# Kernel optimization log

Hardware: AMD Instinct MI355X
Metric: run time of the kernel (lower is better)

## Reference

```python
import jax, jax.numpy as jnp
import numpy as np

D_IN = 1024
D_OUT = 1024
NUM_HEADS = 16
HEAD_DIM = D_OUT // NUM_HEADS


def setup_inputs() -> dict:
    key = jax.random.key(0)
    ks = jax.random.split(key, 6)
    s = 1.0 / np.sqrt(D_IN)
    x = jax.random.normal(ks[0], (2, 2048, D_IN), dtype=jnp.float32)
    Wq = jax.random.uniform(ks[1], (D_IN, D_OUT), jnp.float32, -s, s)
    Wk = jax.random.uniform(ks[2], (D_IN, D_OUT), jnp.float32, -s, s)
    Wv = jax.random.uniform(ks[3], (D_IN, D_OUT), jnp.float32, -s, s)
    Wo = jax.random.uniform(ks[4], (D_OUT, D_OUT), jnp.float32, -s, s)
    bo = jax.random.uniform(ks[5], (D_OUT,), jnp.float32, -s, s)
    return {"x": x, "Wq": Wq, "Wk": Wk, "Wv": Wv, "Wo": Wo, "bo": bo}


def reference(x, Wq, Wk, Wv, Wo, bo):
    b, T, _ = x.shape
    # projections -> [b, heads, T, head_dim]
    def split_heads(y):
        return y.reshape(b, T, NUM_HEADS, HEAD_DIM).transpose(0, 2, 1, 3)
    q = split_heads(x @ Wq)
    k = split_heads(x @ Wk)
    v = split_heads(x @ Wv)
    scores = jnp.einsum("bhqd,bhkd->bhqk", q, k)  # [b,h,T,T]
    causal = jnp.triu(jnp.ones((T, T), dtype=bool), k=1)
    scores = jnp.where(causal, -jnp.inf, scores)
    weights = jax.nn.softmax(scores / np.sqrt(HEAD_DIM), axis=-1)
    # dropout p=0.0 (eval) -> identity
    ctx = jnp.einsum("bhqk,bhkd->bhqd", weights, v)
    ctx = ctx.transpose(0, 2, 1, 3).reshape(b, T, D_OUT)
    return ctx @ Wo + bo
```

## Files before the change

kernel.cpp:

```cpp
#include <hip/hip_runtime.h>
#include <hip/hip_bf16.h>
#include <math.h>

using f32x4  = __attribute__((ext_vector_type(4)))  float;
using f32x16 = __attribute__((ext_vector_type(16))) float;
using s16x8  = __attribute__((ext_vector_type(8)))  short;
using s16x4  = __attribute__((ext_vector_type(4)))  short;

#define HD 64
#define NH 16
#define TT 2048
#define DIN 1024
#define NB 2
#define M_TOK (NB*TT)
#define PADK 40
#define PSTR 36

__device__ __forceinline__ ushort f2b(float f) {
  union { float f; unsigned u; } v; v.f = f;
  unsigned u = v.u;
  return (ushort)((u + 0x7FFFu + ((u >> 16) & 1u)) >> 16);
}

__global__ __launch_bounds__(256) void cvt_f32_bf16(const float* __restrict__ in,
                                                    ushort* __restrict__ out, int n8) {
  int i = blockIdx.x * 256 + threadIdx.x;
  if (i >= n8) return;
  const f32x4* p = (const f32x4*)(in + (size_t)i * 8);
  f32x4 a = p[0], b = p[1];
  s16x8 o;
  o[0]=(short)f2b(a[0]); o[1]=(short)f2b(a[1]); o[2]=(short)f2b(a[2]); o[3]=(short)f2b(a[3]);
  o[4]=(short)f2b(b[0]); o[5]=(short)f2b(b[1]); o[6]=(short)f2b(b[2]); o[7]=(short)f2b(b[3]);
  *(s16x8*)(out + (size_t)i * 8) = o;
}

__global__ __launch_bounds__(256) void transpose_cvt(const float* __restrict__ W,
                                                     ushort* __restrict__ Wt, int K, int N) {
  __shared__ float tile[32][33];
  int nb = blockIdx.x * 32, kb = blockIdx.y * 32;
  int tx = threadIdx.x & 31, ty = threadIdx.x >> 5;
  #pragma unroll
  for (int j = ty; j < 32; j += 8) tile[j][tx] = W[(size_t)(kb + j) * N + nb + tx];
  __syncthreads();
  #pragma unroll
  for (int j = ty; j < 32; j += 8) Wt[(size_t)(nb + j) * K + kb + tx] = f2b(tile[tx][j]);
}

__global__ __launch_bounds__(256) void gemm_qkv(const ushort* __restrict__ Xb,
                                                const ushort* __restrict__ Wt,
                                                ushort* __restrict__ Qb,
                                                ushort* __restrict__ Kb,
                                                ushort* __restrict__ Vt) {
  __shared__ ushort Al[128 * PADK];
  __shared__ ushort Bl[128 * PADK];
  int tid = threadIdx.x, lane = tid & 63, wid = tid >> 6;
  int wr = wid >> 1, wc = wid & 1, g = lane >> 4, c = lane & 15;
  int m0 = blockIdx.y * 128, n0 = blockIdx.x * 128;
  f32x4 acc[4][4] = {};
  for (int k0 = 0; k0 < DIN; k0 += 32) {
    __syncthreads();
    #pragma unroll
    for (int j = 0; j < 2; ++j) {
      int ci = tid + j * 256;
      int row = ci >> 2, part = ci & 3;
      *(s16x8*)&Al[row * PADK + part * 8] =
          *(const s16x8*)&Xb[(size_t)(m0 + row) * DIN + k0 + part * 8];
      *(s16x8*)&Bl[row * PADK + part * 8] =
          *(const s16x8*)&Wt[(size_t)(n0 + row) * DIN + k0 + part * 8];
    }
    __syncthreads();
    s16x8 af[4], bfr[4];
    #pragma unroll
    for (int i = 0; i < 4; ++i) {
      af[i]  = *(const s16x8*)&Al[(wr * 64 + i * 16 + c) * PADK + g * 8];
      bfr[i] = *(const s16x8*)&Bl[(wc * 64 + i * 16 + c) * PADK + g * 8];
    }
    #pragma unroll
    for (int i = 0; i < 4; ++i)
      #pragma unroll
      for (int jn = 0; jn < 4; ++jn)
        acc[i][jn] = __builtin_amdgcn_mfma_f32_16x16x32_bf16(af[i], bfr[jn], acc[i][jn], 0, 0, 0);
  }
  #pragma unroll
  for (int i = 0; i < 4; ++i)
    #pragma unroll
    for (int jn = 0; jn < 4; ++jn) {
      int mrow = m0 + wr * 64 + i * 16 + g * 4;
      int n = n0 + wc * 64 + jn * 16 + c;
      int b = mrow >> 11, t = mrow & (TT - 1);
      int which = n >> 10, nn = n & 1023, h = nn >> 6, d = nn & 63;
      size_t bh = (size_t)(b * NH + h);
      if (which == 2) {
        s16x4 pk;
        pk[0]=(short)f2b(acc[i][jn][0]); pk[1]=(short)f2b(acc[i][jn][1]);
        pk[2]=(short)f2b(acc[i][jn][2]); pk[3]=(short)f2b(acc[i][jn][3]);
        *(s16x4*)&Vt[(bh * HD + d) * TT + t] = pk;
      } else {
        float sc = (which == 0) ? 0.125f * 1.44269504f : 1.0f;
        ushort* dst = (which == 0) ? &Qb[(bh * TT + t) * HD + d]
                                   : &Kb[(bh * TT + t) * HD + d];
        #pragma unroll
        for (int r = 0; r < 4; ++r) dst[(size_t)r * HD] = f2b(acc[i][jn][r] * sc);
      }
    }
}

__global__ __launch_bounds__(256) void attn_fwd(const ushort* __restrict__ Qb,
                                                const ushort* __restrict__ Kb,
                                                const ushort* __restrict__ Vt,
                                                ushort* __restrict__ Ctx) {
  __shared__ __align__(16) char smem[35840];
  int bh = blockIdx.y;
  int qc = (gridDim.x - 1) - blockIdx.x;
  int q0 = qc * 32;
  const ushort* Qh = Qb + (size_t)bh * TT * HD;
  const ushort* Kh = Kb + (size_t)bh * TT * HD;
  const ushort* Vh = Vt + (size_t)bh * HD * TT;
  int tid = threadIdx.x, lane = tid & 63, w = tid >> 6;
  int hi = lane >> 5, c32 = lane & 31;
  int q_abs = q0 + c32;
  int nt = qc + 1;

  ushort* pw = (ushort*)smem + w * (32 * PSTR);

  s16x8 qf[4];
  #pragma unroll
  for (int s = 0; s < 4; ++s)
    qf[s] = *(const s16x8*)&Qh[(size_t)q_abs * HD + s * 16 + 8 * hi];

  f32x16 cA[2] = {};
  float m = -INFINITY, l = 0.f;

  s16x8 kfc[4];
  {
    int tt = (w < nt) ? w : 0;
    #pragma unroll
    for (int s = 0; s < 4; ++s)
      kfc[s] = *(const s16x8*)&Kh[(size_t)(tt * 32 + c32) * HD + s * 16 + 8 * hi];
  }

  for (int t = w; t < nt; t += 4) {
    int kv0 = t * 32;
    int tn = (t + 4 < nt) ? (t + 4) : t;
    s16x8 kfn[4];
    #pragma unroll
    for (int s = 0; s < 4; ++s)
      kfn[s] = *(const s16x8*)&Kh[(size_t)(tn * 32 + c32) * HD + s * 16 + 8 * hi];

    f32x16 S = {};
    #pragma unroll
    for (int s = 0; s < 4; ++s)
      S = __builtin_amdgcn_mfma_f32_32x32x16_bf16(kfc[s], qf[s], S, 0, 0, 0);
    #pragma unroll
    for (int r = 0; r < 16; ++r) {
      int kv_abs = kv0 + (r & 3) + 8 * (r >> 2) + 4 * hi;
      S[r] = (kv_abs > q_abs) ? -INFINITY : S[r];
    }
    float mx[8];
    #pragma unroll
    for (int i = 0; i < 8; ++i) mx[i] = fmaxf(S[2 * i], S[2 * i + 1]);
    #pragma unroll
    for (int i = 0; i < 4; ++i) mx[i] = fmaxf(mx[i], mx[i + 4]);
    mx[0] = fmaxf(fmaxf(mx[0], mx[2]), fmaxf(mx[1], mx[3]));
    float tmax = fmaxf(mx[0], __shfl_xor(mx[0], 32));
    float mnew = fmaxf(m, tmax);
    float alpha = exp2f(m - mnew);
    float p[16];
    #pragma unroll
    for (int r = 0; r < 16; ++r) p[r] = exp2f(S[r] - mnew);
    float sm[8];
    #pragma unroll
    for (int i = 0; i < 8; ++i) sm[i] = p[2 * i] + p[2 * i + 1];
    #pragma unroll
    for (int i = 0; i < 4; ++i) sm[i] += sm[i + 4];
    float rsum = (sm[0] + sm[2]) + (sm[1] + sm[3]);
    rsum += __shfl_xor(rsum, 32);
    l = l * alpha + rsum;
    m = mnew;
    #pragma unroll
    for (int dt = 0; dt < 2; ++dt)
      #pragma unroll
      for (int r = 0; r < 16; ++r) cA[dt][r] *= alpha;
    #pragma unroll
    for (int j = 0; j < 8; ++j) {
      int kvb = ((2 * j) & 3) + 8 * (j >> 1) + 4 * hi;
      unsigned word = (unsigned)f2b(p[2 * j]) | ((unsigned)f2b(p[2 * j + 1]) << 16);
      *(unsigned*)&pw[c32 * PSTR + kvb] = word;
    }
    asm volatile("s_waitcnt lgkmcnt(0)" ::: "memory");
    #pragma unroll
    for (int ks = 0; ks < 2; ++ks) {
      s16x8 vf0 = *(const s16x8*)&Vh[(size_t)(0 * 32 + c32) * TT + kv0 + ks * 16 + 8 * hi];
      s16x8 vf1 = *(const s16x8*)&Vh[(size_t)(1 * 32 + c32) * TT + kv0 + ks * 16 + 8 * hi];
      s16x8 pf  = *(const s16x8*)&pw[c32 * PSTR + ks * 16 + 8 * hi];
      cA[0] = __builtin_amdgcn_mfma_f32_32x32x16_bf16(vf0, pf, cA[0], 0, 0, 0);
      cA[1] = __builtin_amdgcn_mfma_f32_32x32x16_bf16(vf1, pf, cA[1], 0, 0, 0);
    }
    #pragma unroll
    for (int s = 0; s < 4; ++s) kfc[s] = kfn[s];
  }

  __syncthreads();
  float* ctxb = (float*)smem;
  float* mbuf = (float*)(smem + 34816);
  float* lbuf = mbuf + 128;
  #pragma unroll
  for (int dt = 0; dt < 2; ++dt)
    #pragma unroll
    for (int g4 = 0; g4 < 4; ++g4) {
      f32x4 v = { cA[dt][g4 * 4 + 0], cA[dt][g4 * 4 + 1],
                  cA[dt][g4 * 4 + 2], cA[dt][g4 * 4 + 3] };
      *(f32x4*)&ctxb[(size_t)(w * 32 + c32) * 68 + 32 * dt + 8 * g4 + 4 * hi] = v;
    }
  if (!hi) { mbuf[w * 32 + c32] = m; lbuf[w * 32 + c32] = l; }
  __syncthreads();

  int q = tid >> 3, dg = tid & 7;
  float mw[4];
  #pragma unroll
  for (int ww = 0; ww < 4; ++ww) mw[ww] = mbuf[ww * 32 + q];
  float mG = fmaxf(fmaxf(mw[0], mw[1]), fmaxf(mw[2], mw[3]));
  float lt = 0.f;
  f32x4 a0 = {0.f, 0.f, 0.f, 0.f}, a1 = {0.f, 0.f, 0.f, 0.f};
  #pragma unroll
  for (int ww = 0; ww < 4; ++ww) {
    float e = exp2f(mw[ww] - mG);
    lt += e * lbuf[ww * 32 + q];
    const float* src = &ctxb[(size_t)(ww * 32 + q) * 68 + dg * 8];
    f32x4 u0 = *(const f32x4*)&src[0];
    f32x4 u1 = *(const f32x4*)&src[4];
    #pragma unroll
    for (int j = 0; j < 4; ++j) { a0[j] += e * u0[j]; a1[j] += e * u1[j]; }
  }
  float inv = 1.f / lt;
  int b = bh >> 4, h = bh & 15;
  ushort* dst = &Ctx[((size_t)(b * TT) + q0 + q) * DIN + h * HD + dg * 8];
  s16x8 o;
  #pragma unroll
  for (int j = 0; j < 4; ++j) {
    o[j]     = (short)f2b(a0[j] * inv);
    o[4 + j] = (short)f2b(a1[j] * inv);
  }
  *(s16x8*)dst = o;
}

__global__ __launch_bounds__(256) void gemm_out(const ushort* __restrict__ Cb,
                                                const ushort* __restrict__ Wot,
                                                const float* __restrict__ bo,
                                                float* __restrict__ Out) {
  __shared__ ushort Al[128 * PADK];
  __shared__ ushort Bl[128 * PADK];
  int tid = threadIdx.x, lane = tid & 63, wid = tid >> 6;
  int wr = wid >> 1, wc = wid & 1, g = lane >> 4, c = lane & 15;
  int m0 = blockIdx.y * 128, n0 = blockIdx.x * 128;
  f32x4 acc[4][4] = {};
  for (int k0 = 0; k0 < DIN; k0 += 32) {
    __syncthreads();
    #pragma unroll
    for (int j = 0; j < 2; ++j) {
      int ci = tid + j * 256;
      int row = ci >> 2, part = ci & 3;
      *(s16x8*)&Al[row * PADK + part * 8] =
          *(const s16x8*)&Cb[(size_t)(m0 + row) * DIN + k0 + part * 8];
      *(s16x8*)&Bl[row * PADK + part * 8] =
          *(const s16x8*)&Wot[(size_t)(n0 + row) * DIN + k0 + part * 8];
    }
    __syncthreads();
    s16x8 af[4], bfr[4];
    #pragma unroll
    for (int i = 0; i < 4; ++i) {
      af[i]  = *(const s16x8*)&Al[(wr * 64 + i * 16 + c) * PADK + g * 8];
      bfr[i] = *(const s16x8*)&Bl[(wc * 64 + i * 16 + c) * PADK + g * 8];
    }
    #pragma unroll
    for (int i = 0; i < 4; ++i)
      #pragma unroll
      for (int jn = 0; jn < 4; ++jn)
        acc[i][jn] = __builtin_amdgcn_mfma_f32_16x16x32_bf16(af[i], bfr[jn], acc[i][jn], 0, 0, 0);
  }
  #pragma unroll
  for (int i = 0; i < 4; ++i)
    #pragma unroll
    for (int jn = 0; jn < 4; ++jn) {
      int mrow = m0 + wr * 64 + i * 16 + g * 4;
      int n = n0 + wc * 64 + jn * 16 + c;
      float bias = bo[n];
      float* dst = &Out[(size_t)mrow * DIN + n];
      #pragma unroll
      for (int r = 0; r < 4; ++r) dst[(size_t)r * DIN] = acc[i][jn][r] + bias;
    }
}

extern "C" void kernel_launch(void* const* d_in, const int* in_sizes, int n_in,
                              void* d_out, int out_size, void* d_ws, size_t ws_size,
                              hipStream_t stream) {
  const float* x  = (const float*)d_in[0];
  const float* Wq = (const float*)d_in[1];
  const float* Wk = (const float*)d_in[2];
  const float* Wv = (const float*)d_in[3];
  const float* Wo = (const float*)d_in[4];
  const float* bo = (const float*)d_in[5];
  float* Out = (float*)d_out;

  char* ws = (char*)d_ws;
  size_t off = 0;
  auto alloc = [&](size_t bytes) -> char* {
    char* p = ws + off;
    off += (bytes + 255) & ~(size_t)255;
    return p;
  };
  ushort* Xb  = (ushort*)alloc((size_t)M_TOK * DIN * 2);
  ushort* Wt3 = (ushort*)alloc((size_t)3 * 1024 * DIN * 2);
  ushort* Wot = (ushort*)alloc((size_t)1024 * 1024 * 2);
  ushort* Qb  = (ushort*)alloc((size_t)NB * NH * TT * HD * 2);
  ushort* Kb  = (ushort*)alloc((size_t)NB * NH * TT * HD * 2);
  ushort* Vt  = (ushort*)alloc((size_t)NB * NH * TT * HD * 2);
  ushort* Cb  = (ushort*)alloc((size_t)M_TOK * DIN * 2);

  cvt_f32_bf16<<<(M_TOK * DIN / 8 + 255) / 256, 256, 0, stream>>>(x, Xb, M_TOK * DIN / 8);
  dim3 tgrid(1024 / 32, 1024 / 32);
  transpose_cvt<<<tgrid, 256, 0, stream>>>(Wq, Wt3,                   1024, 1024);
  transpose_cvt<<<tgrid, 256, 0, stream>>>(Wk, Wt3 + 1024 * 1024,     1024, 1024);
  transpose_cvt<<<tgrid, 256, 0, stream>>>(Wv, Wt3 + 2 * 1024 * 1024, 1024, 1024);
  transpose_cvt<<<tgrid, 256, 0, stream>>>(Wo, Wot,                   1024, 1024);

  gemm_qkv<<<dim3(3072 / 128, M_TOK / 128), 256, 0, stream>>>(Xb, Wt3, Qb, Kb, Vt);
  attn_fwd<<<dim3(TT / 32, NB * NH), 256, 0, stream>>>(Qb, Kb, Vt, Cb);
  gemm_out<<<dim3(1024 / 128, M_TOK / 128), 256, 0, stream>>>(Cb, Wot, bo, Out);
}
```

Before: 275.4 us.

## Shrink attention LDS footprint, add lazy rescale and hardware bf16 packing

The attention kernel's shared memory drops from about 35KB to 11KB, and the cross-wave combine now runs in four passes over a smaller buffer. A launch bound of 4 blocks per CU is added to raise occupancy. The causal mask is applied only on the diagonal tile, the online-softmax rescale is skipped unless the running max grows by more than 8 (in log2 units), V loads are issued before the QK MFMA, and the next K tile is prefetched in place without the kfn copy. Conversions to bf16 use v_cvt_pk_bf16_f32. In exchange, the combine step gains extra barriers, and the lazy rescale relies on p values staying bounded by 2^8.

```diff
diff --git a/kernel.cpp b/kernel.cpp
--- a/kernel.cpp
+++ b/kernel.cpp
@@ -20,6 +20,12 @@
   union { float f; unsigned u; } v; v.f = f;
   unsigned u = v.u;
   return (ushort)((u + 0x7FFFu + ((u >> 16) & 1u)) >> 16);
+}
+
+__device__ __forceinline__ unsigned cvt_pk_bf16(float lo, float hi) {
+  unsigned r;
+  asm("v_cvt_pk_bf16_f32 %0, %1, %2" : "=v"(r) : "v"(lo), "v"(hi));
+  return r;
 }
 
 __global__ __launch_bounds__(256) void cvt_f32_bf16(const float* __restrict__ in,
@@ -105,11 +111,11 @@
     }
 }
 
-__global__ __launch_bounds__(256) void attn_fwd(const ushort* __restrict__ Qb,
-                                                const ushort* __restrict__ Kb,
-                                                const ushort* __restrict__ Vt,
-                                                ushort* __restrict__ Ctx) {
-  __shared__ __align__(16) char smem[35840];
+__global__ __launch_bounds__(256, 4) void attn_fwd(const ushort* __restrict__ Qb,
+                                                   const ushort* __restrict__ Kb,
+                                                   const ushort* __restrict__ Vt,
+                                                   ushort* __restrict__ Ctx) {
+  __shared__ __align__(16) char smem[11264];
   int bh = blockIdx.y;
   int qc = (gridDim.x - 1) - blockIdx.x;
   int q0 = qc * 32;
@@ -141,20 +147,27 @@
 
   for (int t = w; t < nt; t += 4) {
     int kv0 = t * 32;
-    int tn = (t + 4 < nt) ? (t + 4) : t;
-    s16x8 kfn[4];
-    #pragma unroll
-    for (int s = 0; s < 4; ++s)
-      kfn[s] = *(const s16x8*)&Kh[(size_t)(tn * 32 + c32) * HD + s * 16 + 8 * hi];
-
+    s16x8 vf0[2], vf1[2];
+    #pragma unroll
+    for (int ks = 0; ks < 2; ++ks) {
+      vf0[ks] = *(const s16x8*)&Vh[(size_t)c32 * TT + kv0 + ks * 16 + 8 * hi];
+      vf1[ks] = *(const s16x8*)&Vh[(size_t)(32 + c32) * TT + kv0 + ks * 16 + 8 * hi];
+    }
     f32x16 S = {};
     #pragma unroll
     for (int s = 0; s < 4; ++s)
       S = __builtin_amdgcn_mfma_f32_32x32x16_bf16(kfc[s], qf[s], S, 0, 0, 0);
-    #pragma unroll
-    for (int r = 0; r < 16; ++r) {
-      int kv_abs = kv0 + (r & 3) + 8 * (r >> 2) + 4 * hi;
-      S[r] = (kv_abs > q_abs) ? -INFINITY : S[r];
+    if (t + 4 < nt) {
+      #pragma unroll
+      for (int s = 0; s < 4; ++s)
+        kfc[s] = *(const s16x8*)&Kh[(size_t)((t + 4) * 32 + c32) * HD + s * 16 + 8 * hi];
+    }
+    if (t == qc) {
+      #pragma unroll
+      for (int r = 0; r < 16; ++r) {
+        int pat = (r & 3) + 8 * (r >> 2) + 4 * hi;
+        S[r] = (pat > c32) ? -INFINITY : S[r];
+      }
     }
     float mx[8];
     #pragma unroll
@@ -163,85 +176,86 @@
     for (int i = 0; i < 4; ++i) mx[i] = fmaxf(mx[i], mx[i + 4]);
     mx[0] = fmaxf(fmaxf(mx[0], mx[2]), fmaxf(mx[1], mx[3]));
     float tmax = fmaxf(mx[0], __shfl_xor(mx[0], 32));
-    float mnew = fmaxf(m, tmax);
-    float alpha = exp2f(m - mnew);
-    float p[16];
-    #pragma unroll
-    for (int r = 0; r < 16; ++r) p[r] = exp2f(S[r] - mnew);
+    if (__any(tmax > m + 8.f)) {
+      float mnew = fmaxf(m, tmax);
+      float alpha = exp2f(m - mnew);
+      l *= alpha;
+      #pragma unroll
+      for (int dt = 0; dt < 2; ++dt)
+        #pragma unroll
+        for (int r = 0; r < 16; ++r) cA[dt][r] *= alpha;
+      m = mnew;
+    }
+    #pragma unroll
+    for (int r = 0; r < 16; ++r) S[r] = exp2f(S[r] - m);
     float sm[8];
     #pragma unroll
-    for (int i = 0; i < 8; ++i) sm[i] = p[2 * i] + p[2 * i + 1];
+    for (int i = 0; i < 8; ++i) sm[i] = S[2 * i] + S[2 * i + 1];
     #pragma unroll
     for (int i = 0; i < 4; ++i) sm[i] += sm[i + 4];
     float rsum = (sm[0] + sm[2]) + (sm[1] + sm[3]);
     rsum += __shfl_xor(rsum, 32);
-    l = l * alpha + rsum;
-    m = mnew;
-    #pragma unroll
-    for (int dt = 0; dt < 2; ++dt)
-      #pragma unroll
-      for (int r = 0; r < 16; ++r) cA[dt][r] *= alpha;
+    l += rsum;
     #pragma unroll
     for (int j = 0; j < 8; ++j) {
       int kvb = ((2 * j) & 3) + 8 * (j >> 1) + 4 * hi;
-      unsigned word = (unsigned)f2b(p[2 * j]) | ((unsigned)f2b(p[2 * j + 1]) << 16);
-      *(unsigned*)&pw[c32 * PSTR + kvb] = word;
+      *(unsigned*)&pw[c32 * PSTR + kvb] = cvt_pk_bf16(S[2 * j], S[2 * j + 1]);
     }
     asm volatile("s_waitcnt lgkmcnt(0)" ::: "memory");
     #pragma unroll
     for (int ks = 0; ks < 2; ++ks) {
-      s16x8 vf0 = *(const s16x8*)&Vh[(size_t)(0 * 32 + c32) * TT + kv0 + ks * 16 + 8 * hi];
-      s16x8 vf1 = *(const s16x8*)&Vh[(size_t)(1 * 32 + c32) * TT + kv0 + ks * 16 + 8 * hi];
-      s16x8 pf  = *(const s16x8*)&pw[c32 * PSTR + ks * 16 + 8 * hi];
-      cA[0] = __builtin_amdgcn_mfma_f32_32x32x16_bf16(vf0, pf, cA[0], 0, 0, 0);
-      cA[1] = __builtin_amdgcn_mfma_f32_32x32x16_bf16(vf1, pf, cA[1], 0, 0, 0);
-    }
-    #pragma unroll
-    for (int s = 0; s < 4; ++s) kfc[s] = kfn[s];
+      s16x8 pf = *(const s16x8*)&pw[c32 * PSTR + ks * 16 + 8 * hi];
+      cA[0] = __builtin_amdgcn_mfma_f32_32x32x16_bf16(vf0[ks], pf, cA[0], 0, 0, 0);
+      cA[1] = __builtin_amdgcn_mfma_f32_32x32x16_bf16(vf1[ks], pf, cA[1], 0, 0, 0);
+    }
   }
 
   __syncthreads();
-  float* ctxb = (float*)smem;
-  float* mbuf = (float*)(smem + 34816);
-  float* lbuf = mbuf + 128;
-  #pragma unroll
-  for (int dt = 0; dt < 2; ++dt)
-    #pragma unroll
-    for (int g4 = 0; g4 < 4; ++g4) {
-      f32x4 v = { cA[dt][g4 * 4 + 0], cA[dt][g4 * 4 + 1],
-                  cA[dt][g4 * 4 + 2], cA[dt][g4 * 4 + 3] };
-      *(f32x4*)&ctxb[(size_t)(w * 32 + c32) * 68 + 32 * dt + 8 * g4 + 4 * hi] = v;
-    }
-  if (!hi) { mbuf[w * 32 + c32] = m; lbuf[w * 32 + c32] = l; }
+  float* cb = (float*)smem;
+  float* mb = (float*)(smem + 10240);
+  float* lb = mb + 128;
+  if (!hi) { mb[w * 32 + c32] = m; lb[w * 32 + c32] = l; }
   __syncthreads();
 
-  int q = tid >> 3, dg = tid & 7;
-  float mw[4];
-  #pragma unroll
-  for (int ww = 0; ww < 4; ++ww) mw[ww] = mbuf[ww * 32 + q];
-  float mG = fmaxf(fmaxf(mw[0], mw[1]), fmaxf(mw[2], mw[3]));
-  float lt = 0.f;
-  f32x4 a0 = {0.f, 0.f, 0.f, 0.f}, a1 = {0.f, 0.f, 0.f, 0.f};
-  #pragma unroll
-  for (int ww = 0; ww < 4; ++ww) {
-    float e = exp2f(mw[ww] - mG);
-    lt += e * lbuf[ww * 32 + q];
-    const float* src = &ctxb[(size_t)(ww * 32 + q) * 68 + dg * 8];
-    f32x4 u0 = *(const f32x4*)&src[0];
-    f32x4 u1 = *(const f32x4*)&src[4];
-    #pragma unroll
-    for (int j = 0; j < 4; ++j) { a0[j] += e * u0[j]; a1[j] += e * u1[j]; }
-  }
-  float inv = 1.f / lt;
+  int q  = tid >> 3;
+  int dp = (tid & 7) * 2;
+  float ew[4];
+  {
+    float mw[4];
+    #pragma unroll
+    for (int ww = 0; ww < 4; ++ww) mw[ww] = mb[ww * 32 + q];
+    float mG = fmaxf(fmaxf(mw[0], mw[1]), fmaxf(mw[2], mw[3]));
+    float lt = 0.f;
+    #pragma unroll
+    for (int ww = 0; ww < 4; ++ww) {
+      ew[ww] = exp2f(mw[ww] - mG);
+      lt += ew[ww] * lb[ww * 32 + q];
+    }
+    float inv = 1.f / lt;
+    #pragma unroll
+    for (int ww = 0; ww < 4; ++ww) ew[ww] *= inv;
+  }
   int b = bh >> 4, h = bh & 15;
-  ushort* dst = &Ctx[((size_t)(b * TT) + q0 + q) * DIN + h * HD + dg * 8];
-  s16x8 o;
-  #pragma unroll
-  for (int j = 0; j < 4; ++j) {
-    o[j]     = (short)f2b(a0[j] * inv);
-    o[4 + j] = (short)f2b(a1[j] * inv);
-  }
-  *(s16x8*)dst = o;
+  #pragma unroll
+  for (int rd = 0; rd < 4; ++rd) {
+    int dt = rd >> 1, rh = rd & 1;
+    float* dstq = &cb[(size_t)(w * 32 + c32) * 20];
+    f32x4 v0 = { cA[dt][rh * 8 + 0], cA[dt][rh * 8 + 1], cA[dt][rh * 8 + 2], cA[dt][rh * 8 + 3] };
+    f32x4 v1 = { cA[dt][rh * 8 + 4], cA[dt][rh * 8 + 5], cA[dt][rh * 8 + 6], cA[dt][rh * 8 + 7] };
+    *(f32x4*)&dstq[4 * hi]     = v0;
+    *(f32x4*)&dstq[8 + 4 * hi] = v1;
+    __syncthreads();
+    float s0 = 0.f, s1 = 0.f;
+    #pragma unroll
+    for (int ww = 0; ww < 4; ++ww) {
+      const float* src = &cb[(size_t)(ww * 32 + q) * 20 + dp];
+      s0 += ew[ww] * src[0];
+      s1 += ew[ww] * src[1];
+    }
+    int dcol = h * HD + 32 * dt + 16 * rh + dp;
+    *(unsigned*)&Ctx[((size_t)(b * TT) + q0 + q) * DIN + dcol] = cvt_pk_bf16(s0, s1);
+    if (rd < 3) __syncthreads();
+  }
 }
 
 __global__ __launch_bounds__(256) void gemm_out(const ushort* __restrict__ Cb,
```

Result: no change. 275.2 us (-0.1%).
